# Kernel optimization log

Measured on AMD Instinct MI355X. Metric: run time of the kernel, lower is better.

The kernel has to match this reference:

```python
import jax, jax.numpy as jnp
import numpy as np

V, D, H, L, FF, B, S = 32000, 1024, 16, 4, 4096, 2, 1024
DK = D // H
STD = 0.02


def setup_inputs() -> dict:
    key = jax.random.key(0)
    ks = jax.random.split(key, 9)
    emb = jax.random.normal(ks[0], (V, D), jnp.float32) * STD
    w_qkv = jax.random.normal(ks[1], (L, D, 3 * D), jnp.float32) * STD
    w_o = jax.random.normal(ks[2], (L, D, D), jnp.float32) * STD
    w_gate = jax.random.normal(ks[3], (L, D, FF), jnp.float32) * STD
    w_up = jax.random.normal(ks[4], (L, D, FF), jnp.float32) * STD
    w_down = jax.random.normal(ks[5], (L, FF, D), jnp.float32) * STD
    norm1_w = jnp.ones((L, D), jnp.float32)
    norm2_w = jnp.ones((L, D), jnp.float32)
    final_norm_w = jnp.ones((D,), jnp.float32)
    input_ids = jax.random.randint(ks[6], (B, S), 0, V, dtype=jnp.int32)
    return dict(input_ids=input_ids, emb=emb, w_qkv=w_qkv, w_o=w_o,
                norm1_w=norm1_w, norm2_w=norm2_w,
                w_gate=w_gate, w_up=w_up, w_down=w_down,
                final_norm_w=final_norm_w)


def _rms(x, w, eps=1e-8):
    return w * x / jnp.sqrt(jnp.mean(x * x, axis=-1, keepdims=True) + eps)


def _rope_factor(seq_len, dk):
    # original: x_rope = x*cos + x*sin with cos/sin of shape [S, dk/2]
    # (duplicated along the feature dim to make the broadcast well-defined)
    pos = jnp.arange(seq_len, dtype=jnp.float32)
    freqs = jnp.exp(jnp.arange(0, dk, 2, dtype=jnp.float32) * (-jnp.log(10000.0) / dk))
    ang = pos[:, None] * freqs[None, :]                     # [S, dk/2]
    c = jnp.cos(ang); s = jnp.sin(ang)
    return jnp.concatenate([c, c], -1) + jnp.concatenate([s, s], -1)  # [S, dk]


def reference(input_ids, emb, w_qkv, w_o, norm1_w, norm2_w, w_gate, w_up, w_down, final_norm_w):
    b, s = input_ids.shape
    d = emb.shape[1]
    x = emb[input_ids] * jnp.sqrt(jnp.float32(d))           # [B,S,D]
    rope = _rope_factor(s, DK)                              # [S,DK]
    causal = jnp.tril(jnp.ones((s, s), bool))
    scale = 1.0 / jnp.sqrt(jnp.float32(DK))

    def block(x, p):
        wqkv, wo, n1, n2, wg, wu, wd = p
        nx = _rms(x, n1)
        qkv = (nx @ wqkv).reshape(b, s, 3, H, DK).transpose(2, 0, 3, 1, 4)  # [3,B,H,S,DK]
        q, k, v = qkv[0], qkv[1], qkv[2]
        q = q * rope
        k = k * rope
        scores = jnp.einsum('bhsd,bhtd->bhst', q, k) * scale
        scores = jnp.where(causal, scores, jnp.float32(-1e9))
        attn = jax.nn.softmax(scores, axis=-1)
        o = jnp.einsum('bhst,bhtd->bhsd', attn, v)
        o = o.transpose(0, 2, 1, 3).reshape(b, s, d)
        x = x + o @ wo
        nx = _rms(x, n2)
        ff = (jax.nn.silu(nx @ wg) * (nx @ wu)) @ wd
        return x + ff, None

    x, _ = jax.lax.scan(block, x, (w_qkv, w_o, norm1_w, norm2_w, w_gate, w_up, w_down))
    x = _rms(x, final_norm_w)
    logits = x @ emb.T                                      # tied lm_head
    return logits
```

## Files before the change

kernel.cpp:

```cpp
#include <hip/hip_runtime.h>
#include <hip/hip_bf16.h>
#include <math.h>

#define B_ 2
#define S_ 1024
#define D_ 1024
#define H_ 16
#define DK_ 64
#define L_ 4
#define FF_ 4096
#define V_ 32000
#define NT (B_*S_)

typedef __attribute__((ext_vector_type(8))) short short8v;
typedef __attribute__((ext_vector_type(4))) float floatx4;
typedef __hip_bfloat16 bf16;

__device__ inline float b2f(unsigned short u) {
  unsigned v = ((unsigned)u) << 16;
  float f; __builtin_memcpy(&f, &v, 4); return f;
}
__device__ inline unsigned short f2bu(float f) {
  bf16 h = __float2bfloat16(f);
  unsigned short u; __builtin_memcpy(&u, &h, 2); return u;
}

__global__ __launch_bounds__(256) void k_embed(const int* __restrict__ ids,
    const float* __restrict__ emb, float* __restrict__ x) {
  int i = blockIdx.x*256 + threadIdx.x;
  if (i >= NT*D_) return;
  int tok = i >> 10;
  int d = i & 1023;
  x[i] = emb[(size_t)ids[tok]*D_ + d] * 32.0f;
}

__global__ __launch_bounds__(256) void k_rms(const float* __restrict__ x,
    const float* __restrict__ w, bf16* __restrict__ o) {
  int row = blockIdx.x;
  const float* xr = x + (size_t)row*D_;
  float s = 0.f;
  for (int d = threadIdx.x; d < D_; d += 256) { float v = xr[d]; s += v*v; }
  for (int off = 32; off; off >>= 1) s += __shfl_down(s, off);
  __shared__ float red[4];
  __shared__ float inv_s;
  int wid = threadIdx.x >> 6;
  if ((threadIdx.x & 63) == 0) red[wid] = s;
  __syncthreads();
  if (threadIdx.x == 0) {
    float t = red[0]+red[1]+red[2]+red[3];
    inv_s = 1.0f / sqrtf(t * (1.0f/D_) + 1e-8f);
  }
  __syncthreads();
  float inv = inv_s;
  bf16* orow = o + (size_t)row*D_;
  for (int d = threadIdx.x; d < D_; d += 256) orow[d] = __float2bfloat16(w[d]*xr[d]*inv);
}

__global__ __launch_bounds__(256) void k_transpose_cast(const float* __restrict__ src0,
    bf16* __restrict__ dst0, int K, int N, size_t src_stride, size_t dst_stride) {
  const float* src = src0 + blockIdx.z * src_stride;
  bf16* dst = dst0 + blockIdx.z * dst_stride;
  __shared__ float t[64][65];
  int k0 = blockIdx.y*64, n0 = blockIdx.x*64;
  int r  = threadIdx.x >> 4;
  int c4 = (threadIdx.x & 15)*4;
  #pragma unroll
  for (int i = 0; i < 4; ++i) {
    float4 v = *(const float4*)(src + (size_t)(k0 + r + i*16)*N + n0 + c4);
    t[r+i*16][c4] = v.x; t[r+i*16][c4+1] = v.y;
    t[r+i*16][c4+2] = v.z; t[r+i*16][c4+3] = v.w;
  }
  __syncthreads();
  int nn = threadIdx.x >> 2;
  int kc = threadIdx.x & 3;
  #pragma unroll
  for (int i = 0; i < 4; ++i) {
    int kk = kc*4 + i*16;
    ushort4 o;
    o.x = f2bu(t[kk][nn]);   o.y = f2bu(t[kk+1][nn]);
    o.z = f2bu(t[kk+2][nn]); o.w = f2bu(t[kk+3][nn]);
    *(ushort4*)(dst + (size_t)(n0+nn)*K + k0 + kk) = o;
  }
}

__global__ __launch_bounds__(256) void k_cast4(const float* __restrict__ s,
    bf16* __restrict__ d, int n4) {
  int i = blockIdx.x*256 + threadIdx.x;
  if (i >= n4) return;
  float4 v = ((const float4*)s)[i];
  ushort4 o;
  o.x = f2bu(v.x); o.y = f2bu(v.y); o.z = f2bu(v.z); o.w = f2bu(v.w);
  ((ushort4*)d)[i] = o;
}

template<int EPI, bool OUTBF>
__global__ __launch_bounds__(256) void k_mfma_gemm_bt(
    const bf16* __restrict__ A, const bf16* __restrict__ Bt,
    const void* __restrict__ aux, void* __restrict__ Cout,
    int M, int N, int K) {
  const int NM = M >> 7, NN = N >> 7;
  const int wg = blockIdx.x;
  const int grp = wg >> 3, xcd = wg & 7;
  const int mi = grp % NM;
  const int ni = xcd + 8*(grp / NM);
  if (ni >= NN) return;
  const int bm = mi * 128;
  const int bn = ni * 128;

  __shared__ bf16 As[128*32];
  __shared__ bf16 Bs[128*32];
  const int tid  = threadIdx.x;
  const int lane = tid & 63;
  const int wave = tid >> 6;
  const int wm = (wave >> 1) * 64;
  const int wn = (wave & 1) * 64;

  floatx4 acc[4][4] = {};

  for (int k0 = 0; k0 < K; k0 += 32) {
    #pragma unroll
    for (int c = 0; c < 2; ++c) {
      int e = (c*256 + tid) * 8;
      int row = e >> 5, col = e & 31;
      const bf16* ga = A  + (size_t)(bm + row)*K + k0 + col;
      const bf16* gb = Bt + (size_t)(bn + row)*K + k0 + col;
      int ldsoff = (c*256 + wave*64) * 8;
      __builtin_amdgcn_global_load_lds(
        (const __attribute__((address_space(1))) void*)ga,
        (__attribute__((address_space(3))) void*)(As + ldsoff), 16, 0, 0);
      __builtin_amdgcn_global_load_lds(
        (const __attribute__((address_space(1))) void*)gb,
        (__attribute__((address_space(3))) void*)(Bs + ldsoff), 16, 0, 0);
    }
    __syncthreads();
    const int r = lane & 15, kc = lane >> 4;
    short8v a[4], b[4];
    #pragma unroll
    for (int i = 0; i < 4; ++i) {
      a[i] = *(const short8v*)(As + (size_t)(wm + i*16 + r)*32 + kc*8);
      b[i] = *(const short8v*)(Bs + (size_t)(wn + i*16 + r)*32 + kc*8);
    }
    #pragma unroll
    for (int i = 0; i < 4; ++i)
      #pragma unroll
      for (int j = 0; j < 4; ++j)
        acc[i][j] = __builtin_amdgcn_mfma_f32_16x16x32_bf16(a[i], b[j], acc[i][j], 0, 0, 0);
    __syncthreads();
  }

  const int cn = lane & 15, rq = lane >> 4;
  #pragma unroll
  for (int i=0;i<4;i++) {
    #pragma unroll
    for (int j=0;j<4;j++) {
      const int gcol = bn + wn + j*16 + cn;
      float freq = 0.f;
      if constexpr (EPI==2) {
        if (gcol < 2048)
          freq = expf((float)(gcol & 31) * -0.28782313662425574f);
      }
      #pragma unroll
      for (int rr=0; rr<4; ++rr) {
        const int grow = bm + wm + i*16 + rq*4 + rr;
        const size_t off = (size_t)grow*N + gcol;
        float v = acc[i][j][rr];
        if constexpr (EPI==1) v += ((const float*)aux)[off];
        if constexpr (EPI==2) {
          if (gcol < 2048) {
            float sn, cs;
            sincosf((float)(grow & 1023) * freq, &sn, &cs);
            v *= (cs + sn);
          }
        }
        if constexpr (OUTBF) ((bf16*)Cout)[off] = __float2bfloat16(v);
        else                 ((float*)Cout)[off] = v;
      }
    }
  }
}

static inline int remap_grid(int M, int N) {
  int NM = M >> 7, NN = N >> 7;
  int NN8 = (NN + 7) & ~7;
  return NM * NN8;
}

__global__ __launch_bounds__(256) void k_gemm_64(
    const bf16* __restrict__ A, const bf16* __restrict__ Bt,
    const float* __restrict__ res, float* __restrict__ C,
    int M, int N, int K, int lda) {
  const int NN = N >> 7;
  const int nwg = gridDim.x;
  const int id = (blockIdx.x & 7)*(nwg >> 3) + (blockIdx.x >> 3);
  const int mi = id / NN, ni = id % NN;
  const int bm = mi << 6, bn = ni << 7;

  __shared__ bf16 As[64*32];
  __shared__ bf16 Bs[128*32];
  const int tid  = threadIdx.x;
  const int lane = tid & 63;
  const int wave = tid >> 6;
  const int wm = (wave >> 1) * 32;
  const int wn = (wave & 1) * 64;

  floatx4 acc[2][4] = {};

  for (int k0 = 0; k0 < K; k0 += 32) {
    {
      int row = tid >> 2, col = (tid & 3)*8;
      const bf16* ga = A + (size_t)(bm + row)*lda + k0 + col;
      __builtin_amdgcn_global_load_lds(
        (const __attribute__((address_space(1))) void*)ga,
        (__attribute__((address_space(3))) void*)(As + wave*512), 16, 0, 0);
    }
    #pragma unroll
    for (int c = 0; c < 2; ++c) {
      int i = c*256 + tid;
      int row = i >> 2, col = (i & 3)*8;
      const bf16* gb = Bt + (size_t)(bn + row)*K + k0 + col;
      __builtin_amdgcn_global_load_lds(
        (const __attribute__((address_space(1))) void*)gb,
        (__attribute__((address_space(3))) void*)(Bs + (c*256 + wave*64)*8), 16, 0, 0);
    }
    __syncthreads();
    const int r = lane & 15, kc = lane >> 4;
    short8v a[2], b[4];
    #pragma unroll
    for (int i = 0; i < 2; ++i)
      a[i] = *(const short8v*)(As + (size_t)(wm + i*16 + r)*32 + kc*8);
    #pragma unroll
    for (int j = 0; j < 4; ++j)
      b[j] = *(const short8v*)(Bs + (size_t)(wn + j*16 + r)*32 + kc*8);
    #pragma unroll
    for (int i = 0; i < 2; ++i)
      #pragma unroll
      for (int j = 0; j < 4; ++j)
        acc[i][j] = __builtin_amdgcn_mfma_f32_16x16x32_bf16(a[i], b[j], acc[i][j], 0, 0, 0);
    __syncthreads();
  }

  const int cn = lane & 15, rq = lane >> 4;
  #pragma unroll
  for (int i = 0; i < 2; ++i) {
    #pragma unroll
    for (int j = 0; j < 4; ++j) {
      #pragma unroll
      for (int rr = 0; rr < 4; ++rr) {
        int grow = bm + wm + i*16 + rq*4 + rr;
        int gcol = bn + wn + j*16 + cn;
        size_t off = (size_t)grow*N + gcol;
        C[off] = acc[i][j][rr] + res[off];
      }
    }
  }
}

template<bool OUTBF>
__global__ __launch_bounds__(512, 2) void k_gemm256(
    const bf16* __restrict__ A, const bf16* __restrict__ Bt,
    void* __restrict__ C, int M, int N, int K) {
  const int NM = M >> 8;
  const int nwg = gridDim.x;
  const int id = (blockIdx.x & 7)*(nwg >> 3) + (blockIdx.x >> 3);
  const int mi = id % NM, ni = id / NM;
  const int bm = mi << 8, bn = ni << 8;

  __shared__ bf16 As3[3][256*32];
  __shared__ bf16 Bs3[3][256*32];

  const int tid  = threadIdx.x;
  const int lane = tid & 63;
  const int wave = tid >> 6;
  const int wr = wave >> 2;
  const int wc = wave & 3;
  const int fr = lane & 15;
  const int kc = lane >> 4;

  floatx4 acc[8][4] = {};
  const int ntk = K >> 5;

  auto stage_chunk = [&](int kt, int slot, int c) {
    const bf16* Ab = A  + (size_t)bm*K + kt*32;
    const bf16* Bb = Bt + (size_t)bn*K + kt*32;
    int i = c*512 + tid;
    int row = i >> 2, sl = i & 3;
    int gcol = (sl ^ ((row >> 1) & 3)) * 8;
    int ldsoff = (c*512 + wave*64) * 8;
    __builtin_amdgcn_global_load_lds(
      (const __attribute__((address_space(1))) void*)(Ab + (size_t)row*K + gcol),
      (__attribute__((address_space(3))) void*)(&As3[slot][ldsoff]), 16, 0, 0);
    __builtin_amdgcn_global_load_lds(
      (const __attribute__((address_space(1))) void*)(Bb + (size_t)row*K + gcol),
      (__attribute__((address_space(3))) void*)(&Bs3[slot][ldsoff]), 16, 0, 0);
  };

  stage_chunk(0, 0, 0); stage_chunk(0, 0, 1);
  if (ntk > 1) { stage_chunk(1, 1, 0); stage_chunk(1, 1, 1); }

  for (int t = 0; t < ntk; ++t) {
    const int cur = t % 3;
    if (t + 1 < ntk) asm volatile("s_waitcnt vmcnt(4)" ::: "memory");
    else             asm volatile("s_waitcnt vmcnt(0)" ::: "memory");
    __builtin_amdgcn_sched_barrier(0);
    __builtin_amdgcn_s_barrier();
    __builtin_amdgcn_sched_barrier(0);

    const bf16* Ab = As3[cur];
    const bf16* Bb = Bs3[cur];

    short8v a0[4], b[4];
    #pragma unroll
    for (int f = 0; f < 4; ++f) {
      int r = wr*128 + f*16 + fr;
      a0[f] = *(const short8v*)(Ab + r*32 + (kc ^ ((r >> 1) & 3))*8);
    }
    #pragma unroll
    for (int f = 0; f < 4; ++f) {
      int r = wc*64 + f*16 + fr;
      b[f] = *(const short8v*)(Bb + r*32 + (kc ^ ((r >> 1) & 3))*8);
    }
    if (t + 2 < ntk) stage_chunk(t + 2, (t + 2) % 3, 0);
    asm volatile("s_waitcnt lgkmcnt(0)" ::: "memory");
    __builtin_amdgcn_sched_barrier(0);
    __builtin_amdgcn_s_setprio(1);
    #pragma unroll
    for (int f = 0; f < 4; ++f)
      #pragma unroll
      for (int j = 0; j < 4; ++j)
        acc[f][j] = __builtin_amdgcn_mfma_f32_16x16x32_bf16(a0[f], b[j], acc[f][j], 0, 0, 0);
    __builtin_amdgcn_s_setprio(0);
    __builtin_amdgcn_sched_barrier(0);
    __builtin_amdgcn_s_barrier();
    __builtin_amdgcn_sched_barrier(0);

    short8v a1[4];
    #pragma unroll
    for (int f = 0; f < 4; ++f) {
      int r = wr*128 + (f + 4)*16 + fr;
      a1[f] = *(const short8v*)(Ab + r*32 + (kc ^ ((r >> 1) & 3))*8);
    }
    if (t + 2 < ntk) stage_chunk(t + 2, (t + 2) % 3, 1);
    asm volatile("s_waitcnt lgkmcnt(0)" ::: "memory");
    __builtin_amdgcn_sched_barrier(0);
    __builtin_amdgcn_s_setprio(1);
    #pragma unroll
    for (int f = 0; f < 4; ++f)
      #pragma unroll
      for (int j = 0; j < 4; ++j)
        acc[f + 4][j] = __builtin_amdgcn_mfma_f32_16x16x32_bf16(a1[f], b[j], acc[f + 4][j], 0, 0, 0);
    __builtin_amdgcn_s_setprio(0);
    __builtin_amdgcn_sched_barrier(0);
    __builtin_amdgcn_s_barrier();
    __builtin_amdgcn_sched_barrier(0);
  }

  const int cn = lane & 15, rq = lane >> 4;
  #pragma unroll
  for (int f = 0; f < 8; ++f) {
    #pragma unroll
    for (int j = 0; j < 4; ++j) {
      #pragma unroll
      for (int rr = 0; rr < 4; ++rr) {
        int row = bm + wr*128 + f*16 + rq*4 + rr;
        int col = bn + wc*64 + j*16 + cn;
        size_t off = (size_t)row*N + col;
        if constexpr (OUTBF) ((bf16*)C)[off] = __float2bfloat16(acc[f][j][rr]);
        else                 ((float*)C)[off] = acc[f][j][rr];
      }
    }
  }
}

__global__ __launch_bounds__(256) void k_silumul_gu(bf16* __restrict__ gu) {
  int i = blockIdx.x*256 + threadIdx.x;
  if (i >= NT*512) return;
  int row = i >> 9;
  int c8 = (i & 511)*8;
  unsigned short* p = (unsigned short*)gu + (size_t)row*8192 + c8;
  short8v g = *(const short8v*)p;
  short8v u = *(const short8v*)(p + 4096);
  short8v o;
  #pragma unroll
  for (int j = 0; j < 8; ++j) {
    float gf = b2f((unsigned short)g[j]);
    float uf = b2f((unsigned short)u[j]);
    o[j] = (short)f2bu(gf / (1.0f + expf(-gf)) * uf);
  }
  *(short8v*)p = o;
}

__global__ __launch_bounds__(256) void k_vtrans(const bf16* __restrict__ qkvb,
    bf16* __restrict__ vtb) {
  const unsigned short* qkv = (const unsigned short*)qkvb;
  unsigned short* vt = (unsigned short*)vtb;
  const int t0 = blockIdx.x*64, h = blockIdx.y, b = blockIdx.z;
  __shared__ unsigned short t[64][72];
  const int tid = threadIdx.x;
  #pragma unroll
  for (int c = 0; c < 2; ++c) {
    int idx = c*256 + tid;
    int s = idx >> 3, d0 = (idx & 7)*8;
    short8v v = *(const short8v*)(qkv + ((size_t)(b*S_ + t0 + s))*3072 + 2048 + h*DK_ + d0);
    #pragma unroll
    for (int j = 0; j < 8; ++j) t[s][d0+j] = (unsigned short)v[j];
  }
  __syncthreads();
  #pragma unroll
  for (int c = 0; c < 2; ++c) {
    int idx = c*256 + tid;
    int d = idx >> 3, tt0 = (idx & 7)*8;
    short8v o;
    #pragma unroll
    for (int j = 0; j < 8; ++j) o[j] = (short)t[tt0+j][d];
    *(short8v*)(vt + ((size_t)((b*H_ + h)*DK_ + d))*1024 + t0 + tt0) = o;
  }
}

__global__ __launch_bounds__(256) void k_fattn(const bf16* __restrict__ qkvb,
    const bf16* __restrict__ vtb, bf16* __restrict__ outb) {
  const unsigned short* qkv = (const unsigned short*)qkvb;
  const unsigned short* vt  = (const unsigned short*)vtb;
  const int qt = 15 - blockIdx.x;
  const int h = blockIdx.y, b = blockIdx.z;
  const int tid = threadIdx.x, lane = tid & 63, w = tid >> 6;
  const int g = lane >> 4, qn = lane & 15;

  __shared__ unsigned short Ks[64*64];
  __shared__ unsigned short Vs[64*64];
  __shared__ unsigned short Ps[4*16*64];

  const int q0 = qt * 64;
  const int qw0 = q0 + w*16;

  short8v qf[2];
  {
    const unsigned short* qp = qkv + ((size_t)(b*S_ + qw0 + qn))*3072 + h*DK_ + g*8;
    qf[0] = *(const short8v*)qp;
    qf[1] = *(const short8v*)(qp + 32);
  }

  floatx4 o_acc[4] = {};
  float m_run = -1e30f, l_run = 0.f;

  const int ntile = qt + 1;
  for (int it = 0; it < ntile; ++it) {
    const int t0 = it*64;

    {
      const int trow = w*8 + (lane>>3);
      const int oct = (lane&7) ^ (trow&7);
      #pragma unroll
      for (int c = 0; c < 2; ++c) {
        const unsigned short* gk = qkv + ((size_t)(b*S_ + t0 + c*32 + trow))*3072
                                   + 1024 + h*DK_ + oct*8;
        __builtin_amdgcn_global_load_lds(
          (const __attribute__((address_space(1))) void*)gk,
          (__attribute__((address_space(3))) void*)(Ks + c*2048 + w*512), 16, 0, 0);
        const unsigned short* gv = vt + ((size_t)((b*H_ + h)*DK_ + c*32 + trow))*1024
                                   + t0 + oct*8;
        __builtin_amdgcn_global_load_lds(
          (const __attribute__((address_space(1))) void*)gv,
          (__attribute__((address_space(3))) void*)(Vs + c*2048 + w*512), 16, 0, 0);
      }
    }
    __syncthreads();

    floatx4 st[4];
    #pragma unroll
    for (int f = 0; f < 4; ++f) {
      st[f] = (floatx4){0.f,0.f,0.f,0.f};
      int t = f*16 + qn;
      #pragma unroll
      for (int ks = 0; ks < 2; ++ks) {
        int slot = ((ks*4 + g) ^ (t&7)) & 7;
        short8v kf = *(const short8v*)(Ks + t*64 + slot*8);
        st[f] = __builtin_amdgcn_mfma_f32_16x16x32_bf16(kf, qf[ks], st[f], 0,0,0);
      }
    }

    const bool diag = (it == qt);
    float sc[4][4];
    #pragma unroll
    for (int f = 0; f < 4; ++f)
      #pragma unroll
      for (int r = 0; r < 4; ++r) {
        float v = st[f][r]*0.125f;
        if (diag) {
          int tl = f*16 + g*4 + r;
          if (tl > w*16 + qn) v = -1e30f;
        }
        sc[f][r] = v;
      }
    float mx = -1e30f;
    #pragma unroll
    for (int f = 0; f < 4; ++f)
      #pragma unroll
      for (int r = 0; r < 4; ++r) mx = fmaxf(mx, sc[f][r]);
    mx = fmaxf(mx, __shfl_xor(mx, 16));
    mx = fmaxf(mx, __shfl_xor(mx, 32));
    float m_new = fmaxf(m_run, mx);
    float corr = __expf(m_run - m_new);
    m_run = m_new;
    float ls = 0.f;
    #pragma unroll
    for (int f = 0; f < 4; ++f)
      #pragma unroll
      for (int r = 0; r < 4; ++r) {
        float p = __expf(sc[f][r] - m_new);
        sc[f][r] = p;
        ls += p;
      }
    ls += __shfl_xor(ls, 16);
    ls += __shfl_xor(ls, 32);
    l_run = l_run*corr + ls;

    unsigned short* Pw = Ps + w*1024;
    #pragma unroll
    for (int f = 0; f < 4; ++f) {
      unsigned int lo = (unsigned int)f2bu(sc[f][0]) | ((unsigned int)f2bu(sc[f][1]) << 16);
      unsigned int hi = (unsigned int)f2bu(sc[f][2]) | ((unsigned int)f2bu(sc[f][3]) << 16);
      int c16 = f*2 + (g>>1);
      int slot = (c16 ^ (qn&7)) & 7;
      *(uint2*)((char*)Pw + qn*128 + slot*16 + (g&1)*8) = make_uint2(lo, hi);
    }

    #pragma unroll
    for (int r = 0; r < 4; ++r) {
      float cr = __shfl(corr, g*4 + r);
      #pragma unroll
      for (int fd = 0; fd < 4; ++fd) o_acc[fd][r] *= cr;
    }

    short8v pf[2];
    #pragma unroll
    for (int ks = 0; ks < 2; ++ks) {
      int slot = ((ks*4 + g) ^ (qn&7)) & 7;
      pf[ks] = *(const short8v*)(Pw + qn*64 + slot*8);
    }
    #pragma unroll
    for (int fd = 0; fd < 4; ++fd) {
      int d = fd*16 + qn;
      #pragma unroll
      for (int ks = 0; ks < 2; ++ks) {
        int slot = ((ks*4 + g) ^ (d & 7)) & 7;
        short8v vf = *(const short8v*)(Vs + d*64 + slot*8);
        o_acc[fd] = __builtin_amdgcn_mfma_f32_16x16x32_bf16(pf[ks], vf, o_acc[fd], 0,0,0);
      }
    }
    __syncthreads();
  }

  float linv = 1.0f / l_run;
  #pragma unroll
  for (int r = 0; r < 4; ++r) {
    float li = __shfl(linv, g*4 + r);
    int row = qw0 + g*4 + r;
    bf16* op = outb + (size_t)(b*S_ + row)*D_ + h*DK_ + qn;
    #pragma unroll
    for (int fd = 0; fd < 4; ++fd)
      op[fd*16] = __float2bfloat16(o_acc[fd][r] * li);
  }
}

extern "C" void kernel_launch(void* const* d_in, const int* in_sizes, int n_in,
                              void* d_out, int out_size, void* d_ws, size_t ws_size,
                              hipStream_t stream) {
  (void)in_sizes; (void)n_in; (void)out_size; (void)ws_size;
  const int*   ids  = (const int*)d_in[0];
  const float* emb  = (const float*)d_in[1];
  const float* wqkv = (const float*)d_in[2];
  const float* wo   = (const float*)d_in[3];
  const float* n1   = (const float*)d_in[4];
  const float* n2   = (const float*)d_in[5];
  const float* wg   = (const float*)d_in[6];
  const float* wu   = (const float*)d_in[7];
  const float* wd   = (const float*)d_in[8];
  const float* fnw  = (const float*)d_in[9];
  float* out = (float*)d_out;

  char* ws = (char*)d_ws;
  float* x      = (float*)ws;                                   ws += (size_t)NT*D_*4;
  bf16*  nx_bf  = (bf16*)ws;                                    ws += (size_t)NT*D_*2;
  bf16*  att_bf = (bf16*)ws;                                    ws += (size_t)NT*D_*2;
  bf16*  vt_bf  = (bf16*)ws;                                    ws += (size_t)NT*D_*2;
  bf16*  shared = (bf16*)ws;                                    ws += (size_t)NT*8192*2;
  bf16*  emb_bf = (bf16*)ws;                                    ws += (size_t)V_*D_*2;
  bf16*  qkv_bf = shared;
  bf16*  gu     = shared;

  bf16* wsc = (bf16*)d_out;
  bf16* wqkv_t = wsc;
  bf16* wo_t   = wqkv_t + (size_t)L_*3*D_*D_;
  bf16* wgu_t  = wo_t   + (size_t)L_*D_*D_;
  bf16* wd_t   = wgu_t  + (size_t)L_*2*D_*FF_;

  dim3 blk(256);

  {
    dim3 gq(3*D_/64, D_/64, L_);
    k_transpose_cast<<<gq, blk, 0, stream>>>(wqkv, wqkv_t, D_, 3*D_,
        (size_t)D_*3*D_, (size_t)3*D_*D_);
    dim3 go(D_/64, D_/64, L_);
    k_transpose_cast<<<go, blk, 0, stream>>>(wo, wo_t, D_, D_,
        (size_t)D_*D_, (size_t)D_*D_);
    dim3 gg(FF_/64, D_/64, L_);
    k_transpose_cast<<<gg, blk, 0, stream>>>(wg, wgu_t, D_, FF_,
        (size_t)D_*FF_, (size_t)2*D_*FF_);
    k_transpose_cast<<<gg, blk, 0, stream>>>(wu, wgu_t + (size_t)FF_*D_, D_, FF_,
        (size_t)D_*FF_, (size_t)2*D_*FF_);
    dim3 gdn(D_/64, FF_/64, L_);
    k_transpose_cast<<<gdn, blk, 0, stream>>>(wd, wd_t, FF_, D_,
        (size_t)FF_*D_, (size_t)D_*FF_);
  }
  k_cast4<<<(V_*D_/4 + 255)/256, blk, 0, stream>>>(emb, emb_bf, V_*D_/4);

  k_embed<<<(NT*D_+255)/256, blk, 0, stream>>>(ids, emb, x);

  for (int l = 0; l < L_; ++l) {
    k_rms<<<NT, blk, 0, stream>>>(x, n1 + (size_t)l*D_, nx_bf);
    k_mfma_gemm_bt<2,true><<<remap_grid(NT,3*D_), blk, 0, stream>>>(
        nx_bf, wqkv_t + (size_t)l*3*D_*D_, nullptr, qkv_bf, NT, 3*D_, D_);
    dim3 gvt(S_/64, H_, B_);
    k_vtrans<<<gvt, blk, 0, stream>>>(qkv_bf, vt_bf);
    dim3 gattn(16, H_, B_);
    k_fattn<<<gattn, blk, 0, stream>>>(qkv_bf, vt_bf, att_bf);
    k_gemm_64<<<(NT/64)*(D_/128), blk, 0, stream>>>(
        att_bf, wo_t + (size_t)l*D_*D_, x, x, NT, D_, D_, D_);
    k_rms<<<NT, blk, 0, stream>>>(x, n2 + (size_t)l*D_, nx_bf);
    k_gemm256<true><<<(NT/256)*(2*FF_/256), dim3(512), 0, stream>>>(
        nx_bf, wgu_t + (size_t)l*2*D_*FF_, gu, NT, 2*FF_, D_);
    k_silumul_gu<<<(NT*512 + 255)/256, blk, 0, stream>>>(gu);
    k_gemm_64<<<(NT/64)*(D_/128), blk, 0, stream>>>(
        gu, wd_t + (size_t)l*D_*FF_, x, x, NT, D_, FF_, 2*FF_);
  }
  k_rms<<<NT, blk, 0, stream>>>(x, fnw, nx_bf);
  k_gemm256<false><<<(NT/256)*(V_/256), dim3(512), 0, stream>>>(
      nx_bf, emb_bf, out, NT, V_, D_);
}
```

Measured before the change: 1.270 ms.

## Double-buffer K/V tiles in flash attention to prefetch next tile

The flash-attention kernel now keeps two LDS buffers for K and V. It issues the async global-to-LDS load for the next tile before computing on the current one, and waits with explicit vmcnt counts plus raw s_barrier. This is meant to hide global load latency behind the MFMA and softmax work. In exchange it doubles K/V LDS usage, which may reduce occupancy, and it relies on hand-counted vmcnt values being correct.

```diff
diff --git a/kernel.cpp b/kernel.cpp
--- a/kernel.cpp
+++ b/kernel.cpp
@@ -425,8 +425,8 @@
   const int tid = threadIdx.x, lane = tid & 63, w = tid >> 6;
   const int g = lane >> 4, qn = lane & 15;
 
-  __shared__ unsigned short Ks[64*64];
-  __shared__ unsigned short Vs[64*64];
+  __shared__ unsigned short Ks[2*64*64];
+  __shared__ unsigned short Vs[2*64*64];
   __shared__ unsigned short Ps[4*16*64];
 
   const int q0 = qt * 64;
@@ -439,31 +439,45 @@
     qf[1] = *(const short8v*)(qp + 32);
   }
 
+  const int trow = w*8 + (lane>>3);
+  const int oct = (lane&7) ^ (trow&7);
+  auto stageKV = [&](int it, int buf) {
+    const int t0 = it*64;
+    #pragma unroll
+    for (int c = 0; c < 2; ++c) {
+      const unsigned short* gk = qkv + ((size_t)(b*S_ + t0 + c*32 + trow))*3072
+                                 + 1024 + h*DK_ + oct*8;
+      __builtin_amdgcn_global_load_lds(
+        (const __attribute__((address_space(1))) void*)gk,
+        (__attribute__((address_space(3))) void*)(Ks + buf*4096 + c*2048 + w*512), 16, 0, 0);
+      const unsigned short* gv = vt + ((size_t)((b*H_ + h)*DK_ + c*32 + trow))*1024
+                                 + t0 + oct*8;
+      __builtin_amdgcn_global_load_lds(
+        (const __attribute__((address_space(1))) void*)gv,
+        (__attribute__((address_space(3))) void*)(Vs + buf*4096 + c*2048 + w*512), 16, 0, 0);
+    }
+  };
+
   floatx4 o_acc[4] = {};
   float m_run = -1e30f, l_run = 0.f;
 
   const int ntile = qt + 1;
+  stageKV(0, 0);
+  int cur = 0;
+
   for (int it = 0; it < ntile; ++it) {
-    const int t0 = it*64;
-
-    {
-      const int trow = w*8 + (lane>>3);
-      const int oct = (lane&7) ^ (trow&7);
-      #pragma unroll
-      for (int c = 0; c < 2; ++c) {
-        const unsigned short* gk = qkv + ((size_t)(b*S_ + t0 + c*32 + trow))*3072
-                                   + 1024 + h*DK_ + oct*8;
-        __builtin_amdgcn_global_load_lds(
-          (const __attribute__((address_space(1))) void*)gk,
-          (__attribute__((address_space(3))) void*)(Ks + c*2048 + w*512), 16, 0, 0);
-        const unsigned short* gv = vt + ((size_t)((b*H_ + h)*DK_ + c*32 + trow))*1024
-                                   + t0 + oct*8;
-        __builtin_amdgcn_global_load_lds(
-          (const __attribute__((address_space(1))) void*)gv,
-          (__attribute__((address_space(3))) void*)(Vs + c*2048 + w*512), 16, 0, 0);
-      }
-    }
-    __syncthreads();
+    if (it + 1 < ntile) {
+      stageKV(it + 1, cur ^ 1);
+      asm volatile("s_waitcnt vmcnt(4)" ::: "memory");
+    } else {
+      asm volatile("s_waitcnt vmcnt(0)" ::: "memory");
+    }
+    __builtin_amdgcn_sched_barrier(0);
+    __builtin_amdgcn_s_barrier();
+    __builtin_amdgcn_sched_barrier(0);
+
+    const unsigned short* Kc = Ks + cur*4096;
+    const unsigned short* Vc = Vs + cur*4096;
 
     floatx4 st[4];
     #pragma unroll
@@ -473,7 +487,7 @@
       #pragma unroll
       for (int ks = 0; ks < 2; ++ks) {
         int slot = ((ks*4 + g) ^ (t&7)) & 7;
-        short8v kf = *(const short8v*)(Ks + t*64 + slot*8);
+        short8v kf = *(const short8v*)(Kc + t*64 + slot*8);
         st[f] = __builtin_amdgcn_mfma_f32_16x16x32_bf16(kf, qf[ks], st[f], 0,0,0);
       }
     }
@@ -543,11 +557,15 @@
       #pragma unroll
       for (int ks = 0; ks < 2; ++ks) {
         int slot = ((ks*4 + g) ^ (d & 7)) & 7;
-        short8v vf = *(const short8v*)(Vs + d*64 + slot*8);
+        short8v vf = *(const short8v*)(Vc + d*64 + slot*8);
         o_acc[fd] = __builtin_amdgcn_mfma_f32_16x16x32_bf16(pf[ks], vf, o_acc[fd], 0,0,0);
       }
     }
-    __syncthreads();
+
+    __builtin_amdgcn_sched_barrier(0);
+    __builtin_amdgcn_s_barrier();
+    __builtin_amdgcn_sched_barrier(0);
+    cur ^= 1;
   }
 
   float linv = 1.0f / l_run;
```

New measurement: 1.273 ms. No clear change (+0.2%).
